# Kernel tuning notes

Measured on AMD Instinct MI355X. Metric: run time of the kernel, lower is better.

The kernel has to match this reference:

```python
import jax, jax.numpy as jnp
import numpy as np
import math

D = 1024
H = 8
HD = D // H
TEMP = math.sqrt(D)
EPS = 1e-5

def _layernorm(x, g, b):
    mu = jnp.mean(x, axis=-1, keepdims=True)
    var = jnp.var(x, axis=-1, keepdims=True)
    return (x - mu) * jax.lax.rsqrt(var + EPS) * g + b

def setup_inputs() -> dict:
    key = jax.random.key(0)
    ks = jax.random.split(key, 8)
    B, Lq, Lk = 4, 2048, 2048
    Q = jax.random.normal(ks[0], (B, Lq, D), dtype=jnp.float32)
    K = jax.random.normal(ks[1], (B, Lk, D), dtype=jnp.float32)
    V = jax.random.normal(ks[2], (B, Lk, D), dtype=jnp.float32)
    Wq = jax.random.normal(ks[3], (D, D), dtype=jnp.float32) * 0.02
    Wk = jax.random.normal(ks[4], (D, D), dtype=jnp.float32) * 0.02
    Wv = jax.random.normal(ks[5], (D, D), dtype=jnp.float32) * 0.02
    Wo = jax.random.normal(ks[6], (D, D), dtype=jnp.float32) * 0.02
    pre_g = jnp.ones((D,), jnp.float32)
    pre_b = jnp.zeros((D,), jnp.float32)
    ln_g = jnp.ones((D,), jnp.float32)
    ln_b = jnp.zeros((D,), jnp.float32)
    return {"Q": Q, "K": K, "V": V, "Wq": Wq, "Wk": Wk, "Wv": Wv, "Wo": Wo,
            "pre_g": pre_g, "pre_b": pre_b, "ln_g": ln_g, "ln_b": ln_b}

def reference(Q, K, V, Wq, Wk, Wv, Wo, pre_g, pre_b, ln_g, ln_b):
    B, Lq, _ = Q.shape
    Lk = K.shape[1]
    # pre-LN on Q and K only (V untouched, as in original)
    Qn = _layernorm(Q, pre_g, pre_b)
    Kn = _layernorm(K, pre_g, pre_b)
    q = (Qn @ Wq).reshape(B, Lq, H, HD)
    k = (Kn @ Wk).reshape(B, Lk, H, HD)
    v = (V @ Wv).reshape(B, Lk, H, HD)
    scores = jnp.einsum('bqhd,bkhd->bhqk', q, k) / TEMP
    scores = jnp.clip(scores, -10000.0, 10000.0)
    A = jax.nn.softmax(scores, axis=-1)  # dropout = identity in eval
    O = jnp.einsum('bhqk,bkhd->bqhd', A, v).reshape(B, Lq, D)
    O = _layernorm(O, ln_g, ln_b)
    O = O + jax.nn.gelu(O @ Wo, approximate=False)  # residual branch
    return O
```

## Files before the change

### kernel.cpp

```cpp
#include <hip/hip_runtime.h>
#include <math.h>

typedef unsigned short u16;
typedef __bf16 bf16x8 __attribute__((ext_vector_type(8)));
typedef float f32x4 __attribute__((ext_vector_type(4)));

union B8u { uint4 u; bf16x8 v; u16 s[8]; };

__device__ __forceinline__ u16 f2bf(float f){
  unsigned u = __float_as_uint(f);
  u += 0x7fffu + ((u >> 16) & 1u);
  return (u16)(u >> 16);
}
__device__ __forceinline__ bf16x8 ld8(const u16* p){
  B8u x; x.u = *(const uint4*)p; return x.v;
}
__device__ __forceinline__ void glds16(const u16* g, u16* l){
  __builtin_amdgcn_global_load_lds(
      (const __attribute__((address_space(1))) void*)g,
      (__attribute__((address_space(3))) void*)l, 16, 0, 0);
}

__global__ void wcast_k(const float* __restrict__ Wq, const float* __restrict__ Wk,
                        const float* __restrict__ Wv, const float* __restrict__ Wo,
                        u16* __restrict__ Tq, u16* __restrict__ Tk,
                        u16* __restrict__ Tv, u16* __restrict__ To){
  const float* W; u16* T;
  switch(blockIdx.z){
    case 0: W = Wq; T = Tq; break;
    case 1: W = Wk; T = Tk; break;
    case 2: W = Wv; T = Tv; break;
    default: W = Wo; T = To; break;
  }
  __shared__ u16 tile[32][33];
  int tx = threadIdx.x & 31, ty = threadIdx.x >> 5;
  int n0 = blockIdx.x * 32, k0 = blockIdx.y * 32;
  for(int i = ty; i < 32; i += 8)
    tile[i][tx] = f2bf(W[(size_t)(k0 + i) * 1024 + n0 + tx]);
  __syncthreads();
  for(int i = ty; i < 32; i += 8)
    T[(size_t)(n0 + i) * 1024 + k0 + tx] = tile[tx][i];
}

__device__ __forceinline__ void ln_core(const float* __restrict__ X,
                                        u16* __restrict__ Y, float* __restrict__ Yf,
                                        const float* __restrict__ g,
                                        const float* __restrict__ bb,
                                        int doLN, int row, int t, float* red){
  float4 v = ((const float4*)(X + (size_t)row * 1024))[t];
  float o0 = v.x, o1 = v.y, o2 = v.z, o3 = v.w;
  if(doLN){
    float s  = o0 + o1 + o2 + o3;
    float ss = o0*o0 + o1*o1 + o2*o2 + o3*o3;
    for(int o = 32; o > 0; o >>= 1){
      s  += __shfl_down(s,  o, 64);
      ss += __shfl_down(ss, o, 64);
    }
    if((t & 63) == 0){ red[t >> 6] = s; red[4 + (t >> 6)] = ss; }
    __syncthreads();
    s  = red[0] + red[1] + red[2] + red[3];
    ss = red[4] + red[5] + red[6] + red[7];
    float mu  = s * (1.f/1024.f);
    float var = ss * (1.f/1024.f) - mu*mu;
    float rs  = rsqrtf(var + 1e-5f);
    float4 gg = ((const float4*)g)[t];
    float4 bv = ((const float4*)bb)[t];
    o0 = (o0 - mu) * rs * gg.x + bv.x;
    o1 = (o1 - mu) * rs * gg.y + bv.y;
    o2 = (o2 - mu) * rs * gg.z + bv.z;
    o3 = (o3 - mu) * rs * gg.w + bv.w;
  }
  if(Yf){
    float4 w; w.x=o0; w.y=o1; w.z=o2; w.w=o3;
    ((float4*)(Yf + (size_t)row * 1024))[t] = w;
  }
  ushort4 u;
  u.x = f2bf(o0); u.y = f2bf(o1); u.z = f2bf(o2); u.w = f2bf(o3);
  ((ushort4*)(Y + (size_t)row * 1024))[t] = u;
}

__global__ void ln3_cast(const float* __restrict__ Q, const float* __restrict__ K,
                         const float* __restrict__ V,
                         u16* __restrict__ QN, u16* __restrict__ KN, u16* __restrict__ VB,
                         const float* __restrict__ g, const float* __restrict__ bb){
  __shared__ float red[8];
  const float* X; u16* Y; int doLN = 1;
  switch(blockIdx.y){
    case 0: X = Q; Y = QN; break;
    case 1: X = K; Y = KN; break;
    default: X = V; Y = VB; doLN = 0; break;
  }
  ln_core(X, Y, nullptr, g, bb, doLN, blockIdx.x, threadIdx.x, red);
}

__global__ void ln_post(const float* __restrict__ X, u16* __restrict__ Y,
                        float* __restrict__ Yf,
                        const float* __restrict__ g, const float* __restrict__ bb){
  __shared__ float red[8];
  ln_core(X, Y, Yf, g, bb, 1, blockIdx.x, threadIdx.x, red);
}

template<int MODE>
__device__ __forceinline__ void gemm_core(
  const u16* __restrict__ A, const u16* __restrict__ Bt,
  u16* __restrict__ Obf, float* __restrict__ Of32, const float* __restrict__ Resid,
  int m0, int n0, int ldC, float oscale, u16* as, u16* bs)
{
  const int K = 1024;
  int t = threadIdx.x;
  int wave = t >> 6, lane = t & 63, quad = lane >> 4, l16 = lane & 15;
  int wm = (wave >> 1) * 64, wn = (wave & 1) * 64;
  int srow = t >> 3;
  f32x4 acc[4][4] = {};
  for(int k0 = 0; k0 < K; k0 += 64){
    __syncthreads();
    for(int p = 0; p < 4; p++){
      int r = p*32 + srow;
      int c = (t & 7) ^ (r & 7);
      glds16(A  + (size_t)(m0 + r) * K + k0 + c*8, as + p*2048 + wave*512);
      glds16(Bt + (size_t)(n0 + r) * K + k0 + c*8, bs + p*2048 + wave*512);
    }
    __syncthreads();
    bf16x8 af[2][4], bfr[2][4];
    for(int kk = 0; kk < 2; kk++)
      for(int mt = 0; mt < 4; mt++){
        int ra = wm + mt*16 + l16;
        af[kk][mt]  = ld8(&as[ra*64 + (((kk*4 + quad) ^ (ra & 7)) * 8)]);
        int rb = wn + mt*16 + l16;
        bfr[kk][mt] = ld8(&bs[rb*64 + (((kk*4 + quad) ^ (rb & 7)) * 8)]);
      }
    for(int kk = 0; kk < 2; kk++)
      for(int mt = 0; mt < 4; mt++)
        for(int nt = 0; nt < 4; nt++)
          acc[mt][nt] = __builtin_amdgcn_mfma_f32_16x16x32_bf16(af[kk][mt], bfr[kk][nt], acc[mt][nt], 0, 0, 0);
  }
  for(int mt = 0; mt < 4; mt++)
    for(int nt = 0; nt < 4; nt++){
      int col = n0 + wn + nt*16 + l16;
      for(int r = 0; r < 4; r++){
        int row = m0 + wm + mt*16 + quad*4 + r;
        size_t idx = (size_t)row * ldC + col;
        float v = acc[mt][nt][r];
        if(MODE == 0){
          Obf[idx] = f2bf(v * oscale);
        } else {
          float ge = 0.5f * v * (1.0f + erff(v * 0.70710678118f));
          Of32[idx] = Resid[idx] + ge;
        }
      }
    }
}

__global__ __launch_bounds__(256,3) void qkv_gemm(
  const u16* __restrict__ QN, const u16* __restrict__ KN, const u16* __restrict__ VB,
  const u16* __restrict__ WTq, const u16* __restrict__ WTk, const u16* __restrict__ WTv,
  u16* __restrict__ QP, u16* __restrict__ KP, u16* __restrict__ VT, float qscale)
{
  __shared__ u16 as[128*64];
  __shared__ u16 bs[128*64];
  int bx = blockIdx.x;
  int z = bx % 3, id = bx / 3;
  if(z == 0){
    gemm_core<0>(QN, WTq, QP, nullptr, nullptr, (id >> 3)*128, (id & 7)*128, 1024, qscale, as, bs);
  } else if(z == 1){
    gemm_core<0>(KN, WTk, KP, nullptr, nullptr, (id >> 3)*128, (id & 7)*128, 1024, 1.0f, as, bs);
  } else {
    gemm_core<0>(WTv, VB, VT, nullptr, nullptr, (id & 7)*128, (id >> 3)*128, 8192, 1.0f, as, bs);
  }
}

__global__ __launch_bounds__(256,3) void out_gemm(
  const u16* __restrict__ A, const u16* __restrict__ Bt,
  float* __restrict__ Of32, const float* __restrict__ Resid)
{
  __shared__ u16 as[128*64];
  __shared__ u16 bs[128*64];
  gemm_core<1>(A, Bt, nullptr, Of32, Resid, blockIdx.x*128, blockIdx.y*128, 1024, 1.0f, as, bs);
}

__global__ __launch_bounds__(256,2) void flash_k(
  const u16* __restrict__ Qp, const u16* __restrict__ Kp, const u16* __restrict__ VT,
  float* __restrict__ Oout)
{
  __shared__ u16 ks[64*128];
  __shared__ u16 vts[128*64];
  __shared__ u16 ps[128][72];
  int t = threadIdx.x, wave = t >> 6, lane = t & 63, quad = lane >> 4, l16 = lane & 15;
  int l = blockIdx.x;
  int xcd = l & 7, i = l >> 3;
  int bh = xcd + 8 * (i & 3);
  int qt = i >> 2;
  int b = bh >> 3, h = bh & 7;
  size_t rowbase = (size_t)b * 2048;
  int colbase = h * 128;
  int wq = wave * 32;

  bf16x8 aq[2][4];
  for(int mt = 0; mt < 2; mt++){
    const u16* qrow = Qp + (rowbase + qt*128 + wq + mt*16 + l16) * 1024 + colbase + quad*8;
    for(int kk = 0; kk < 4; kk++) aq[mt][kk] = ld8(qrow + kk*32);
  }

  float l_i[2][4] = {};
  f32x4 oacc[2][8] = {};

  int krow = t >> 4;
  int kchunk = lane & 15;
  int vrow = t >> 3;
  int vchunk = lane & 7;

  for(int p = 0; p < 4; p++){
    int kr = p*16 + krow;
    int ck = kchunk ^ (kr & 15);
    glds16(Kp + (rowbase + kr) * 1024 + colbase + ck*8, ks + p*2048 + wave*512);
  }
  for(int p = 0; p < 4; p++){
    int vr = p*32 + vrow;
    int cv = vchunk ^ (vr & 7);
    glds16(VT + (size_t)(colbase + vr) * 8192 + rowbase + cv*8,
           vts + p*2048 + wave*512);
  }
  __syncthreads();

  for(int kt = 0; kt < 2048; kt += 64){
    f32x4 s[2][4] = {};
    for(int ct = 0; ct < 4; ct++)
      for(int kk = 0; kk < 4; kk++){
        bf16x8 bb = ld8(&ks[(ct*16 + l16)*128 + (((kk*4 + quad) ^ l16) * 8)]);
        s[0][ct] = __builtin_amdgcn_mfma_f32_16x16x32_bf16(aq[0][kk], bb, s[0][ct], 0, 0, 0);
        s[1][ct] = __builtin_amdgcn_mfma_f32_16x16x32_bf16(aq[1][kk], bb, s[1][ct], 0, 0, 0);
      }
    for(int mt = 0; mt < 2; mt++)
      for(int ct = 0; ct < 4; ct++)
        for(int r = 0; r < 4; r++)
          s[mt][ct][r] = __builtin_amdgcn_exp2f(s[mt][ct][r]);
    for(int mt = 0; mt < 2; mt++)
      for(int r = 0; r < 4; r++){
        l_i[mt][r] += (s[mt][0][r] + s[mt][1][r]) + (s[mt][2][r] + s[mt][3][r]);
        for(int ct = 0; ct < 4; ct++){
          unsigned u = __float_as_uint(s[mt][ct][r]) + 0x8000u;
          ps[wq + mt*16 + quad*4 + r][ct*16 + l16] = (u16)(u >> 16);
        }
      }
    __syncthreads();
    if(kt + 64 < 2048){
      for(int p = 0; p < 4; p++){
        int kr = p*16 + krow;
        int ck = kchunk ^ (kr & 15);
        glds16(Kp + (rowbase + kt + 64 + kr) * 1024 + colbase + ck*8,
               ks + p*2048 + wave*512);
      }
    }
    bf16x8 pa[2][2];
    for(int mt = 0; mt < 2; mt++){
      pa[mt][0] = ld8(&ps[wq + mt*16 + l16][quad*8]);
      pa[mt][1] = ld8(&ps[wq + mt*16 + l16][32 + quad*8]);
    }
    for(int dt = 0; dt < 8; dt++){
      int vrw = (dt*16 + l16)*64;
      int r7 = l16 & 7;
      bf16x8 b0 = ld8(&vts[vrw + ((quad ^ r7) * 8)]);
      oacc[0][dt] = __builtin_amdgcn_mfma_f32_16x16x32_bf16(pa[0][0], b0, oacc[0][dt], 0, 0, 0);
      oacc[1][dt] = __builtin_amdgcn_mfma_f32_16x16x32_bf16(pa[1][0], b0, oacc[1][dt], 0, 0, 0);
      bf16x8 b1 = ld8(&vts[vrw + (((4 + quad) ^ r7) * 8)]);
      oacc[0][dt] = __builtin_amdgcn_mfma_f32_16x16x32_bf16(pa[0][1], b1, oacc[0][dt], 0, 0, 0);
      oacc[1][dt] = __builtin_amdgcn_mfma_f32_16x16x32_bf16(pa[1][1], b1, oacc[1][dt], 0, 0, 0);
    }
    __syncthreads();
    if(kt + 64 < 2048){
      for(int p = 0; p < 4; p++){
        int vr = p*32 + vrow;
        int cv = vchunk ^ (vr & 7);
        glds16(VT + (size_t)(colbase + vr) * 8192 + rowbase + kt + 64 + cv*8,
               vts + p*2048 + wave*512);
      }
    }
  }
  for(int mt = 0; mt < 2; mt++){
    float rinv[4];
    for(int r = 0; r < 4; r++){
      float lv = l_i[mt][r];
      for(int o = 1; o < 16; o <<= 1) lv += __shfl_xor(lv, o, 64);
      rinv[r] = 1.f / lv;
    }
    for(int dt = 0; dt < 8; dt++){
      int col = colbase + dt*16 + l16;
      for(int r = 0; r < 4; r++){
        size_t row = rowbase + qt*128 + wq + mt*16 + quad*4 + r;
        Oout[row * 1024 + col] = oacc[mt][dt][r] * rinv[r];
      }
    }
  }
}

extern "C" void kernel_launch(void* const* d_in, const int* in_sizes, int n_in,
                              void* d_out, int out_size, void* d_ws, size_t ws_size,
                              hipStream_t stream){
  (void)in_sizes; (void)n_in; (void)out_size; (void)ws_size;
  const float* Q    = (const float*)d_in[0];
  const float* K    = (const float*)d_in[1];
  const float* V    = (const float*)d_in[2];
  const float* Wq   = (const float*)d_in[3];
  const float* Wk   = (const float*)d_in[4];
  const float* Wv   = (const float*)d_in[5];
  const float* Wo   = (const float*)d_in[6];
  const float* pre_g = (const float*)d_in[7];
  const float* pre_b = (const float*)d_in[8];
  const float* ln_g  = (const float*)d_in[9];
  const float* ln_b  = (const float*)d_in[10];
  float* Out = (float*)d_out;
  char* ws = (char*)d_ws;
  const size_t MB = 1024 * 1024;
  u16* WTq = (u16*)(ws + 0*MB);
  u16* WTk = (u16*)(ws + 2*MB);
  u16* WTv = (u16*)(ws + 4*MB);
  u16* WTo = (u16*)(ws + 6*MB);
  u16* QN  = (u16*)(ws + 8*MB);
  u16* KN  = (u16*)(ws + 24*MB);
  u16* VB  = (u16*)(ws + 40*MB);
  u16* QP  = (u16*)(ws + 56*MB);
  u16* KP  = (u16*)(ws + 72*MB);
  u16* VT  = (u16*)(ws + 88*MB);
  float* OLN  = (float*)(ws + 8*MB);
  u16*   OLNb = (u16*)(ws + 40*MB);

  const float qscale = 0.03125f * 1.44269504089f;

  wcast_k<<<dim3(32,32,4), 256, 0, stream>>>(Wq,Wk,Wv,Wo, WTq,WTk,WTv,WTo);
  ln3_cast<<<dim3(8192,3), 256, 0, stream>>>(Q, K, V, QN, KN, VB, pre_g, pre_b);
  qkv_gemm<<<1536, 256, 0, stream>>>(QN, KN, VB, WTq, WTk, WTv, QP, KP, VT, qscale);
  flash_k<<<512, 256, 0, stream>>>(QP, KP, VT, Out);
  ln_post<<<8192, 256, 0, stream>>>(Out, OLNb, OLN, ln_g, ln_b);
  out_gemm<<<dim3(64,8), 256, 0, stream>>>(OLNb, WTo, Out, OLN);
}
```

Baseline: 357.3 us.

## Split flash attention across 8 waves of 16 query rows with MFMA priority

Reworks the flash attention kernel from 4 waves each owning 32 query rows to 8 waves each owning 16 rows, using 512-thread blocks. The K/V tile loads are redistributed across the larger block. s_setprio is raised around the MFMA phases. The goal is more waves in flight to hide LDS and exp latency, at the cost of losing the reuse of each K/V fragment across two row tiles, which doubles LDS reads per MFMA.

```diff
diff --git a/kernel.cpp b/kernel.cpp
--- a/kernel.cpp
+++ b/kernel.cpp
@@ -178,7 +178,7 @@
   gemm_core<1>(A, Bt, nullptr, Of32, Resid, blockIdx.x*128, blockIdx.y*128, 1024, 1.0f, as, bs);
 }
 
-__global__ __launch_bounds__(256,2) void flash_k(
+__global__ __launch_bounds__(512,4) void flash_k(
   const u16* __restrict__ Qp, const u16* __restrict__ Kp, const u16* __restrict__ VT,
   float* __restrict__ Oout)
 {
@@ -193,102 +193,96 @@
   int b = bh >> 3, h = bh & 7;
   size_t rowbase = (size_t)b * 2048;
   int colbase = h * 128;
-  int wq = wave * 32;
-
-  bf16x8 aq[2][4];
-  for(int mt = 0; mt < 2; mt++){
-    const u16* qrow = Qp + (rowbase + qt*128 + wq + mt*16 + l16) * 1024 + colbase + quad*8;
-    for(int kk = 0; kk < 4; kk++) aq[mt][kk] = ld8(qrow + kk*32);
-  }
-
-  float l_i[2][4] = {};
-  f32x4 oacc[2][8] = {};
+  int wq = wave * 16;
+
+  bf16x8 aq[4];
+  {
+    const u16* qrow = Qp + (rowbase + qt*128 + wq + l16) * 1024 + colbase + quad*8;
+    for(int kk = 0; kk < 4; kk++) aq[kk] = ld8(qrow + kk*32);
+  }
+
+  float l_i[4] = {};
+  f32x4 oacc[8] = {};
 
   int krow = t >> 4;
   int kchunk = lane & 15;
   int vrow = t >> 3;
   int vchunk = lane & 7;
 
-  for(int p = 0; p < 4; p++){
-    int kr = p*16 + krow;
+  for(int p = 0; p < 2; p++){
+    int kr = p*32 + krow;
     int ck = kchunk ^ (kr & 15);
-    glds16(Kp + (rowbase + kr) * 1024 + colbase + ck*8, ks + p*2048 + wave*512);
-  }
-  for(int p = 0; p < 4; p++){
-    int vr = p*32 + vrow;
+    glds16(Kp + (rowbase + kr) * 1024 + colbase + ck*8, ks + p*4096 + wave*512);
+  }
+  for(int p = 0; p < 2; p++){
+    int vr = p*64 + vrow;
     int cv = vchunk ^ (vr & 7);
     glds16(VT + (size_t)(colbase + vr) * 8192 + rowbase + cv*8,
-           vts + p*2048 + wave*512);
+           vts + p*4096 + wave*512);
   }
   __syncthreads();
 
   for(int kt = 0; kt < 2048; kt += 64){
-    f32x4 s[2][4] = {};
+    f32x4 s[4] = {};
+    __builtin_amdgcn_s_setprio(1);
     for(int ct = 0; ct < 4; ct++)
       for(int kk = 0; kk < 4; kk++){
         bf16x8 bb = ld8(&ks[(ct*16 + l16)*128 + (((kk*4 + quad) ^ l16) * 8)]);
-        s[0][ct] = __builtin_amdgcn_mfma_f32_16x16x32_bf16(aq[0][kk], bb, s[0][ct], 0, 0, 0);
-        s[1][ct] = __builtin_amdgcn_mfma_f32_16x16x32_bf16(aq[1][kk], bb, s[1][ct], 0, 0, 0);
-      }
-    for(int mt = 0; mt < 2; mt++)
-      for(int ct = 0; ct < 4; ct++)
-        for(int r = 0; r < 4; r++)
-          s[mt][ct][r] = __builtin_amdgcn_exp2f(s[mt][ct][r]);
-    for(int mt = 0; mt < 2; mt++)
-      for(int r = 0; r < 4; r++){
-        l_i[mt][r] += (s[mt][0][r] + s[mt][1][r]) + (s[mt][2][r] + s[mt][3][r]);
-        for(int ct = 0; ct < 4; ct++){
-          unsigned u = __float_as_uint(s[mt][ct][r]) + 0x8000u;
-          ps[wq + mt*16 + quad*4 + r][ct*16 + l16] = (u16)(u >> 16);
-        }
-      }
+        s[ct] = __builtin_amdgcn_mfma_f32_16x16x32_bf16(aq[kk], bb, s[ct], 0, 0, 0);
+      }
+    __builtin_amdgcn_s_setprio(0);
+    for(int ct = 0; ct < 4; ct++)
+      for(int r = 0; r < 4; r++)
+        s[ct][r] = __builtin_amdgcn_exp2f(s[ct][r]);
+    for(int r = 0; r < 4; r++){
+      l_i[r] += (s[0][r] + s[1][r]) + (s[2][r] + s[3][r]);
+      for(int ct = 0; ct < 4; ct++){
+        unsigned u = __float_as_uint(s[ct][r]) + 0x8000u;
+        ps[wq + quad*4 + r][ct*16 + l16] = (u16)(u >> 16);
+      }
+    }
     __syncthreads();
     if(kt + 64 < 2048){
-      for(int p = 0; p < 4; p++){
-        int kr = p*16 + krow;
+      for(int p = 0; p < 2; p++){
+        int kr = p*32 + krow;
         int ck = kchunk ^ (kr & 15);
         glds16(Kp + (rowbase + kt + 64 + kr) * 1024 + colbase + ck*8,
-               ks + p*2048 + wave*512);
-      }
-    }
-    bf16x8 pa[2][2];
-    for(int mt = 0; mt < 2; mt++){
-      pa[mt][0] = ld8(&ps[wq + mt*16 + l16][quad*8]);
-      pa[mt][1] = ld8(&ps[wq + mt*16 + l16][32 + quad*8]);
-    }
+               ks + p*4096 + wave*512);
+      }
+    }
+    bf16x8 pa0 = ld8(&ps[wq + l16][quad*8]);
+    bf16x8 pa1 = ld8(&ps[wq + l16][32 + quad*8]);
+    __builtin_amdgcn_s_setprio(1);
     for(int dt = 0; dt < 8; dt++){
       int vrw = (dt*16 + l16)*64;
       int r7 = l16 & 7;
       bf16x8 b0 = ld8(&vts[vrw + ((quad ^ r7) * 8)]);
-      oacc[0][dt] = __builtin_amdgcn_mfma_f32_16x16x32_bf16(pa[0][0], b0, oacc[0][dt], 0, 0, 0);
-      oacc[1][dt] = __builtin_amdgcn_mfma_f32_16x16x32_bf16(pa[1][0], b0, oacc[1][dt], 0, 0, 0);
+      oacc[dt] = __builtin_amdgcn_mfma_f32_16x16x32_bf16(pa0, b0, oacc[dt], 0, 0, 0);
       bf16x8 b1 = ld8(&vts[vrw + (((4 + quad) ^ r7) * 8)]);
-      oacc[0][dt] = __builtin_amdgcn_mfma_f32_16x16x32_bf16(pa[0][1], b1, oacc[0][dt], 0, 0, 0);
-      oacc[1][dt] = __builtin_amdgcn_mfma_f32_16x16x32_bf16(pa[1][1], b1, oacc[1][dt], 0, 0, 0);
-    }
+      oacc[dt] = __builtin_amdgcn_mfma_f32_16x16x32_bf16(pa1, b1, oacc[dt], 0, 0, 0);
+    }
+    __builtin_amdgcn_s_setprio(0);
     __syncthreads();
     if(kt + 64 < 2048){
-      for(int p = 0; p < 4; p++){
-        int vr = p*32 + vrow;
+      for(int p = 0; p < 2; p++){
+        int vr = p*64 + vrow;
         int cv = vchunk ^ (vr & 7);
         glds16(VT + (size_t)(colbase + vr) * 8192 + rowbase + kt + 64 + cv*8,
-               vts + p*2048 + wave*512);
-      }
-    }
-  }
-  for(int mt = 0; mt < 2; mt++){
-    float rinv[4];
+               vts + p*4096 + wave*512);
+      }
+    }
+  }
+  float rinv[4];
+  for(int r = 0; r < 4; r++){
+    float lv = l_i[r];
+    for(int o = 1; o < 16; o <<= 1) lv += __shfl_xor(lv, o, 64);
+    rinv[r] = 1.f / lv;
+  }
+  for(int dt = 0; dt < 8; dt++){
+    int col = colbase + dt*16 + l16;
     for(int r = 0; r < 4; r++){
-      float lv = l_i[mt][r];
-      for(int o = 1; o < 16; o <<= 1) lv += __shfl_xor(lv, o, 64);
-      rinv[r] = 1.f / lv;
-    }
-    for(int dt = 0; dt < 8; dt++){
-      int col = colbase + dt*16 + l16;
-      for(int r = 0; r < 4; r++){
-        size_t row = rowbase + qt*128 + wq + mt*16 + quad*4 + r;
-        Oout[row * 1024 + col] = oacc[mt][dt][r] * rinv[r];
-      }
+      size_t row = rowbase + qt*128 + wq + quad*4 + r;
+      Oout[row * 1024 + col] = oacc[dt][r] * rinv[r];
     }
   }
 }
@@ -329,7 +323,7 @@
   wcast_k<<<dim3(32,32,4), 256, 0, stream>>>(Wq,Wk,Wv,Wo, WTq,WTk,WTv,WTo);
   ln3_cast<<<dim3(8192,3), 256, 0, stream>>>(Q, K, V, QN, KN, VB, pre_g, pre_b);
   qkv_gemm<<<1536, 256, 0, stream>>>(QN, KN, VB, WTq, WTk, WTv, QP, KP, VT, qscale);
-  flash_k<<<512, 256, 0, stream>>>(QP, KP, VT, Out);
+  flash_k<<<512, 512, 0, stream>>>(QP, KP, VT, Out);
   ln_post<<<8192, 256, 0, stream>>>(Out, OLNb, OLN, ln_g, ln_b);
   out_gemm<<<dim3(64,8), 256, 0, stream>>>(OLNb, WTo, Out, OLN);
 }
```

New measurement: 356.6 us. About the same (-0.2%).
